# Kernel optimization log

Measured on AMD Instinct MI355X. Metric: run time of the kernel, lower is better.

The kernel has to match this reference:

```python
import jax, jax.numpy as jnp
import numpy as np

IN, H, STEPS = 4, 64, 5

def setup_inputs() -> dict:
    key = jax.random.key(0)
    ks = jax.random.split(key, 12)
    s = 1.0 / np.sqrt(H)
    def u(k, shape):
        return jax.random.uniform(k, shape, jnp.float32, -s, s)
    return {
        "x":    jax.random.normal(ks[0], (4096, 512, IN), jnp.float32),
        "Wih0": u(ks[1], (4 * H, IN)),
        "Whh0": u(ks[2], (4 * H, H)),
        "bih0": u(ks[3], (4 * H,)),
        "bhh0": u(ks[4], (4 * H,)),
        "Wih1": u(ks[5], (4 * H, H)),
        "Whh1": u(ks[6], (4 * H, H)),
        "bih1": u(ks[7], (4 * H,)),
        "bhh1": u(ks[8], (4 * H,)),
        "Wfc":  u(ks[9], (IN * STEPS, H)),
        "bfc":  u(ks[10], (IN * STEPS,)),
    }

def _lstm_layer(x, Wih, Whh, bih, bhh, collect):
    # x: [B, T, in]; PyTorch gate order: i, f, g, o
    B = x.shape[0]
    xg = jnp.einsum('bti,gi->tbg', x, Wih) + bih  # precompute input gates [T,B,4H]
    h0 = jnp.zeros((B, H), x.dtype)
    c0 = jnp.zeros((B, H), x.dtype)

    def step(carry, xg_t):
        h, c = carry
        gates = xg_t + h @ Whh.T + bhh  # [B,4H]
        i, f, g, o = jnp.split(gates, 4, axis=-1)
        i = jax.nn.sigmoid(i); f = jax.nn.sigmoid(f)
        g = jnp.tanh(g);       o = jax.nn.sigmoid(o)
        c = f * c + i * g
        h = o * jnp.tanh(c)
        return (h, c), (h if collect else None)

    (h_last, _), ys = jax.lax.scan(step, (h0, c0), xg)
    return ys, h_last  # ys: [T,B,H] (or None)

def reference(x, Wih0, Whh0, bih0, bhh0, Wih1, Whh1, bih1, bhh1, Wfc, bfc):
    ys1, _ = _lstm_layer(x, Wih0, Whh0, bih0, bhh0, collect=True)   # [T,B,H]
    x2 = jnp.transpose(ys1, (1, 0, 2))                               # [B,T,H]
    _, h_last = _lstm_layer(x2, Wih1, Whh1, bih1, bhh1, collect=False)
    out = h_last @ Wfc.T + bfc                                       # [B, IN*STEPS]
    return out.reshape(-1, STEPS, IN)
```

## Files before the change

### kernel.cpp

```cpp
#include <hip/hip_runtime.h>
#include <hip/hip_bf16.h>
#include <cstdint>

#define BLOCK 512
#define BT 16
#define RS_H 136
#define RS_F 68
#define XS   2052

typedef __attribute__((ext_vector_type(8))) short bf16x8;
typedef __attribute__((ext_vector_type(4))) float f32x4;
typedef __attribute__((ext_vector_type(2))) float f32x2;
typedef __attribute__((ext_vector_type(2))) unsigned int u32x2;

#define LOG2E 1.44269504f

static __device__ __forceinline__ float exp2_fast(float x) {
#if __has_builtin(__builtin_amdgcn_exp2f)
    return __builtin_amdgcn_exp2f(x);
#else
    return __expf(x * 0.69314718056f);
#endif
}
static __device__ __forceinline__ float rcp_fast(float x) {
    return __builtin_amdgcn_rcpf(x);
}
static __device__ __forceinline__ unsigned short f2bf(float f) {
    union { float f; unsigned u; } v; v.f = f;
    unsigned r = v.u + 0x7fffu + ((v.u >> 16) & 1u);
    return (unsigned short)(r >> 16);
}
static __device__ __forceinline__ bf16x8 load_wfrag(const float* __restrict__ w, int off, float scale) {
    union { bf16x8 v; unsigned short s[8]; } u;
#pragma unroll
    for (int j = 0; j < 8; ++j) u.s[j] = f2bf(w[off + j] * scale);
    return u.v;
}

extern "C" __global__ void __launch_bounds__(BLOCK, 2)
lstm_fused5(const float* __restrict__ x,
            const float* __restrict__ Wih0, const float* __restrict__ Whh0,
            const float* __restrict__ bih0, const float* __restrict__ bhh0,
            const float* __restrict__ Wih1, const float* __restrict__ Whh1,
            const float* __restrict__ bih1, const float* __restrict__ bhh1,
            const float* __restrict__ Wfc,  const float* __restrict__ bfc,
            float* __restrict__ out)
{
    __shared__ unsigned short hbuf[2][BT * RS_H];
    __shared__ float hfin[BT * RS_F];
    __shared__ unsigned short xlds[BT * XS + 8];

    const int tid   = threadIdx.x;
    const int b0    = blockIdx.x * BT;
    const int lane  = tid & 63;
    const int wv    = tid >> 6;
    const int layer = wv >> 2;
    const int cb    = (wv & 3) * 16;
    const int n16   = lane & 15;
    const int quad  = lane >> 4;

    for (int i = tid; i < 2 * BT * RS_H; i += BLOCK)
        ((unsigned short*)hbuf)[i] = 0;

    for (int i = tid; i < BT * 512; i += BLOCK) {
        const int r = i >> 9, t = i & 511;
        const f32x4 xv = *(const f32x4*)(x + ((size_t)(b0 + r) * 2048 + t * 4));
        const unsigned lo = (unsigned)f2bf(xv[0]) | ((unsigned)f2bf(xv[1]) << 16);
        const unsigned hi = (unsigned)f2bf(xv[2]) | ((unsigned)f2bf(xv[3]) << 16);
        *(u32x2*)&xlds[r * XS + t * 4] = (u32x2){lo, hi};
    }
    if (tid <= BT) {
        const int off = (tid < BT) ? tid * XS + 2048 : BT * XS;
        *(u32x2*)&xlds[off] = (u32x2){0u, 0u};
    }

    const float gsc[4] = {-LOG2E, -LOG2E, 2.0f * LOG2E, -LOG2E};

    bf16x8 wf[4][4];
    f32x4  biasv[4];
    if (layer == 0) {
#pragma unroll
        for (int g = 0; g < 4; ++g) {
            const int gc = g * 64 + cb + n16;
            const float s = gsc[g];
            wf[g][0] = load_wfrag(Whh0 + gc * 64, quad * 8, s);
            wf[g][1] = load_wfrag(Whh0 + gc * 64, 32 + quad * 8, s);
            union { bf16x8 v; unsigned short s_[8]; } u;
#pragma unroll
            for (int c = 0; c < 4; ++c)
                u.s_[c] = (quad == 0) ? f2bf(Wih0[gc * 4 + c] * s) : (unsigned short)0;
            u.s_[4] = 0; u.s_[5] = 0; u.s_[6] = 0; u.s_[7] = 0;
            wf[g][2] = u.v;
            const float b = (bih0[gc] + bhh0[gc]) * s;
            biasv[g] = (f32x4){b, b, b, b};
        }
    } else {
#pragma unroll
        for (int g = 0; g < 4; ++g) {
            const int gc = g * 64 + cb + n16;
            const float s = gsc[g];
            wf[g][0] = load_wfrag(Wih1 + gc * 64, quad * 8, s);
            wf[g][1] = load_wfrag(Wih1 + gc * 64, 32 + quad * 8, s);
            wf[g][2] = load_wfrag(Whh1 + gc * 64, quad * 8, s);
            wf[g][3] = load_wfrag(Whh1 + gc * 64, 32 + quad * 8, s);
            const float b = (bih1[gc] + bhh1[gc]) * s;
            biasv[g] = (f32x4){b, b, b, b};
        }
    }

    float cst[4] = {0.f, 0.f, 0.f, 0.f};

    int xoff = (quad == 0) ? n16 * XS : BT * XS;
    const int xadv = (quad == 0) ? 4 : 0;
    const int rbase = n16 * RS_H;

    const f32x2 onev  = {1.0f, 1.0f};
    const f32x2 k2l   = {2.0f * LOG2E, 2.0f * LOG2E};
    const f32x2 km2l  = {-2.0f * LOG2E, -2.0f * LOG2E};
    const f32x2 cclmp = {60.0f, 60.0f};

    __syncthreads();

    for (int it = 0; it <= 512; ++it) {
        const unsigned short* rb = &hbuf[(it + 1) & 1][0];
        unsigned short*       wb = &hbuf[it & 1][0];

        const bf16x8 a0 = *(const bf16x8*)(rb + rbase + quad * 8);
        const bf16x8 a1 = *(const bf16x8*)(rb + rbase + 32 + quad * 8);

        f32x4 acc[4];
        if (layer == 0) {
            const u32x2 xr = *(const u32x2*)&xlds[xoff];
            xoff += xadv;
            union { bf16x8 v; unsigned u[4]; } ax;
            ax.u[0] = xr.x; ax.u[1] = xr.y; ax.u[2] = 0u; ax.u[3] = 0u;
            const bf16x8 a2 = ax.v;
#pragma unroll
            for (int g = 0; g < 4; ++g) {
                acc[g] = __builtin_amdgcn_mfma_f32_16x16x32_bf16(a0, wf[g][0], biasv[g], 0, 0, 0);
                acc[g] = __builtin_amdgcn_mfma_f32_16x16x32_bf16(a1, wf[g][1], acc[g], 0, 0, 0);
                acc[g] = __builtin_amdgcn_mfma_f32_16x16x32_bf16(a2, wf[g][2], acc[g], 0, 0, 0);
            }
        } else {
            const bf16x8 a2 = *(const bf16x8*)(rb + rbase + 64 + quad * 8);
            const bf16x8 a3 = *(const bf16x8*)(rb + rbase + 96 + quad * 8);
#pragma unroll
            for (int g = 0; g < 4; ++g) {
                acc[g] = __builtin_amdgcn_mfma_f32_16x16x32_bf16(a0, wf[g][0], biasv[g], 0, 0, 0);
                acc[g] = __builtin_amdgcn_mfma_f32_16x16x32_bf16(a1, wf[g][1], acc[g], 0, 0, 0);
                acc[g] = __builtin_amdgcn_mfma_f32_16x16x32_bf16(a2, wf[g][2], acc[g], 0, 0, 0);
                acc[g] = __builtin_amdgcn_mfma_f32_16x16x32_bf16(a3, wf[g][3], acc[g], 0, 0, 0);
            }
        }

        const bool active = layer ? (it >= 1) : (it < 512);
        if (active) {
#pragma unroll
            for (int p = 0; p < 2; ++p) {
                const f32x2 ei = {exp2_fast(acc[0][2*p]), exp2_fast(acc[0][2*p+1])};
                const f32x2 ef = {exp2_fast(acc[1][2*p]), exp2_fast(acc[1][2*p+1])};
                const f32x2 eg = {exp2_fast(acc[2][2*p]), exp2_fast(acc[2][2*p+1])};
                const f32x2 eo = {exp2_fast(acc[3][2*p]), exp2_fast(acc[3][2*p+1])};

                const f32x2 t2 = __builtin_elementwise_fma(eg, k2l, km2l);
                const f32x2 d1 = (eg + onev) * (ei + onev);
                const f32x2 df = ef + onev;
                const f32x2 r1 = {rcp_fast(d1[0]), rcp_fast(d1[1])};
                const f32x2 fv = {rcp_fast(df[0]), rcp_fast(df[1])};
                const f32x2 P  = t2 * r1;

                f32x2 cp = {cst[2*p], cst[2*p+1]};
                f32x2 c2 = __builtin_elementwise_fma(fv, cp, P);
                c2 = __builtin_elementwise_min(c2, cclmp);
                cst[2*p] = c2[0]; cst[2*p+1] = c2[1];

                const f32x2 ec = {exp2_fast(c2[0]), exp2_fast(c2[1])};
                const f32x2 d2 = (ec + onev) * (eo + onev);
                const f32x2 r2 = {rcp_fast(d2[0]), rcp_fast(d2[1])};
                const f32x2 h  = (ec - onev) * r2;

                const int row0 = quad * 4 + 2 * p;
                unsigned short* wp = wb + row0 * RS_H + layer * 64 + cb + n16;
                union { __hip_bfloat162 b; unsigned short s[2]; } hb;
                hb.b = __float22bfloat162_rn(make_float2(h[0], h[1]));
                wp[0]    = hb.s[0];
                wp[RS_H] = hb.s[1];
                if (layer == 1 && it == 512) {
                    hfin[row0 * RS_F + cb + n16]       = h[0];
                    hfin[(row0 + 1) * RS_F + cb + n16] = h[1];
                }
            }
        }
        __syncthreads();
    }

    if (tid < BT * 20) {
        const int m = tid / 20, k = tid % 20;
        float acc = bfc[k];
#pragma unroll 8
        for (int j = 0; j < 64; ++j)
            acc += hfin[m * RS_F + j] * Wfc[k * 64 + j];
        out[(b0 + m) * 20 + k] = acc;
    }
}

extern "C" void kernel_launch(void* const* d_in, const int* in_sizes, int n_in,
                              void* d_out, int out_size, void* d_ws, size_t ws_size,
                              hipStream_t stream)
{
    (void)in_sizes; (void)n_in; (void)d_ws; (void)ws_size; (void)out_size;
    const float* xp    = (const float*)d_in[0];
    const float* Wih0p = (const float*)d_in[1];
    const float* Whh0p = (const float*)d_in[2];
    const float* bih0p = (const float*)d_in[3];
    const float* bhh0p = (const float*)d_in[4];
    const float* Wih1p = (const float*)d_in[5];
    const float* Whh1p = (const float*)d_in[6];
    const float* bih1p = (const float*)d_in[7];
    const float* bhh1p = (const float*)d_in[8];
    const float* Wfcp  = (const float*)d_in[9];
    const float* bfcp  = (const float*)d_in[10];

    lstm_fused5<<<dim3(256), dim3(BLOCK), 0, stream>>>(
        xp, Wih0p, Whh0p, bih0p, bhh0p, Wih1p, Whh1p, bih1p, bhh1p,
        Wfcp, bfcp, (float*)d_out);
}
```

Baseline: 432.8 us.

## Transpose MFMA operands, vectorize h stores, merge reciprocals, unroll loop by two

```diff
diff --git a/kernel.cpp b/kernel.cpp
--- a/kernel.cpp
+++ b/kernel.cpp
@@ -12,6 +12,7 @@
 typedef __attribute__((ext_vector_type(4))) float f32x4;
 typedef __attribute__((ext_vector_type(2))) float f32x2;
 typedef __attribute__((ext_vector_type(2))) unsigned int u32x2;
+typedef __attribute__((ext_vector_type(4))) unsigned int u32x4;
 
 #define LOG2E 1.44269504f
 
@@ -38,7 +39,7 @@
 }
 
 extern "C" __global__ void __launch_bounds__(BLOCK, 2)
-lstm_fused5(const float* __restrict__ x,
+lstm_fused6(const float* __restrict__ x,
             const float* __restrict__ Wih0, const float* __restrict__ Whh0,
             const float* __restrict__ bih0, const float* __restrict__ bhh0,
             const float* __restrict__ Wih1, const float* __restrict__ Whh1,
@@ -91,8 +92,10 @@
                 u.s_[c] = (quad == 0) ? f2bf(Wih0[gc * 4 + c] * s) : (unsigned short)0;
             u.s_[4] = 0; u.s_[5] = 0; u.s_[6] = 0; u.s_[7] = 0;
             wf[g][2] = u.v;
-            const float b = (bih0[gc] + bhh0[gc]) * s;
-            biasv[g] = (f32x4){b, b, b, b};
+            const int gb = g * 64 + cb + quad * 4;
+#pragma unroll
+            for (int r = 0; r < 4; ++r)
+                biasv[g][r] = (bih0[gb + r] + bhh0[gb + r]) * s;
         }
     } else {
 #pragma unroll
@@ -103,8 +106,10 @@
             wf[g][1] = load_wfrag(Wih1 + gc * 64, 32 + quad * 8, s);
             wf[g][2] = load_wfrag(Whh1 + gc * 64, quad * 8, s);
             wf[g][3] = load_wfrag(Whh1 + gc * 64, 32 + quad * 8, s);
-            const float b = (bih1[gc] + bhh1[gc]) * s;
-            biasv[g] = (f32x4){b, b, b, b};
+            const int gb = g * 64 + cb + quad * 4;
+#pragma unroll
+            for (int r = 0; r < 4; ++r)
+                biasv[g][r] = (bih1[gb + r] + bhh1[gb + r]) * s;
         }
     }
 
@@ -112,7 +117,14 @@
 
     int xoff = (quad == 0) ? n16 * XS : BT * XS;
     const int xadv = (quad == 0) ? 4 : 0;
-    const int rbase = n16 * RS_H;
+
+    const int rbase = n16 * RS_H + quad * 8;
+    const int wbase = n16 * RS_H + layer * 64 + cb + quad * 4;
+    const unsigned short* __restrict__ rdp0 = &hbuf[1][rbase];
+    const unsigned short* __restrict__ rdp1 = &hbuf[0][rbase];
+    unsigned short* __restrict__ wrp0 = &hbuf[0][wbase];
+    unsigned short* __restrict__ wrp1 = &hbuf[1][wbase];
+    float* __restrict__ hfp = &hfin[n16 * RS_F + cb + quad * 4];
 
     const f32x2 onev  = {1.0f, 1.0f};
     const f32x2 k2l   = {2.0f * LOG2E, 2.0f * LOG2E};
@@ -121,40 +133,44 @@
 
     __syncthreads();
 
-    for (int it = 0; it <= 512; ++it) {
-        const unsigned short* rb = &hbuf[(it + 1) & 1][0];
-        unsigned short*       wb = &hbuf[it & 1][0];
-
-        const bf16x8 a0 = *(const bf16x8*)(rb + rbase + quad * 8);
-        const bf16x8 a1 = *(const bf16x8*)(rb + rbase + 32 + quad * 8);
-
+    auto step = [&](const unsigned short* __restrict__ rp,
+                    unsigned short* __restrict__ wp,
+                    bool l0act, bool l1act, bool fin) __attribute__((always_inline)) {
         f32x4 acc[4];
         if (layer == 0) {
-            const u32x2 xr = *(const u32x2*)&xlds[xoff];
-            xoff += xadv;
-            union { bf16x8 v; unsigned u[4]; } ax;
-            ax.u[0] = xr.x; ax.u[1] = xr.y; ax.u[2] = 0u; ax.u[3] = 0u;
-            const bf16x8 a2 = ax.v;
-#pragma unroll
-            for (int g = 0; g < 4; ++g) {
-                acc[g] = __builtin_amdgcn_mfma_f32_16x16x32_bf16(a0, wf[g][0], biasv[g], 0, 0, 0);
-                acc[g] = __builtin_amdgcn_mfma_f32_16x16x32_bf16(a1, wf[g][1], acc[g], 0, 0, 0);
-                acc[g] = __builtin_amdgcn_mfma_f32_16x16x32_bf16(a2, wf[g][2], acc[g], 0, 0, 0);
+            if (l0act) {
+                const bf16x8 s0 = *(const bf16x8*)(rp);
+                const bf16x8 s1 = *(const bf16x8*)(rp + 32);
+                const u32x2 xr = *(const u32x2*)&xlds[xoff];
+                xoff += xadv;
+                const u32x4 xt = {xr.x, xr.y, 0u, 0u};
+                const bf16x8 sx = __builtin_bit_cast(bf16x8, xt);
+#pragma unroll
+                for (int g = 0; g < 4; ++g) {
+                    acc[g] = __builtin_amdgcn_mfma_f32_16x16x32_bf16(wf[g][0], s0, biasv[g], 0, 0, 0);
+                    acc[g] = __builtin_amdgcn_mfma_f32_16x16x32_bf16(wf[g][1], s1, acc[g], 0, 0, 0);
+                    acc[g] = __builtin_amdgcn_mfma_f32_16x16x32_bf16(wf[g][2], sx, acc[g], 0, 0, 0);
+                }
             }
         } else {
-            const bf16x8 a2 = *(const bf16x8*)(rb + rbase + 64 + quad * 8);
-            const bf16x8 a3 = *(const bf16x8*)(rb + rbase + 96 + quad * 8);
-#pragma unroll
-            for (int g = 0; g < 4; ++g) {
-                acc[g] = __builtin_amdgcn_mfma_f32_16x16x32_bf16(a0, wf[g][0], biasv[g], 0, 0, 0);
-                acc[g] = __builtin_amdgcn_mfma_f32_16x16x32_bf16(a1, wf[g][1], acc[g], 0, 0, 0);
-                acc[g] = __builtin_amdgcn_mfma_f32_16x16x32_bf16(a2, wf[g][2], acc[g], 0, 0, 0);
-                acc[g] = __builtin_amdgcn_mfma_f32_16x16x32_bf16(a3, wf[g][3], acc[g], 0, 0, 0);
+            if (l1act) {
+                const bf16x8 s0 = *(const bf16x8*)(rp);
+                const bf16x8 s1 = *(const bf16x8*)(rp + 32);
+                const bf16x8 s2 = *(const bf16x8*)(rp + 64);
+                const bf16x8 s3 = *(const bf16x8*)(rp + 96);
+#pragma unroll
+                for (int g = 0; g < 4; ++g) {
+                    acc[g] = __builtin_amdgcn_mfma_f32_16x16x32_bf16(wf[g][0], s0, biasv[g], 0, 0, 0);
+                    acc[g] = __builtin_amdgcn_mfma_f32_16x16x32_bf16(wf[g][1], s1, acc[g], 0, 0, 0);
+                    acc[g] = __builtin_amdgcn_mfma_f32_16x16x32_bf16(wf[g][2], s2, acc[g], 0, 0, 0);
+                    acc[g] = __builtin_amdgcn_mfma_f32_16x16x32_bf16(wf[g][3], s3, acc[g], 0, 0, 0);
+                }
             }
         }
-
-        const bool active = layer ? (it >= 1) : (it < 512);
-        if (active) {
+        const bool act = layer ? l1act : l0act;
+        if (act) {
+            unsigned hw0 = 0, hw1 = 0;
+            float hf0 = 0.f, hf1 = 0.f, hf2 = 0.f, hf3 = 0.f;
 #pragma unroll
             for (int p = 0; p < 2; ++p) {
                 const f32x2 ei = {exp2_fast(acc[0][2*p]), exp2_fast(acc[0][2*p+1])};
@@ -165,9 +181,10 @@
                 const f32x2 t2 = __builtin_elementwise_fma(eg, k2l, km2l);
                 const f32x2 d1 = (eg + onev) * (ei + onev);
                 const f32x2 df = ef + onev;
-                const f32x2 r1 = {rcp_fast(d1[0]), rcp_fast(d1[1])};
-                const f32x2 fv = {rcp_fast(df[0]), rcp_fast(df[1])};
-                const f32x2 P  = t2 * r1;
+                const f32x2 pr = d1 * df;
+                const f32x2 R  = {rcp_fast(pr[0]), rcp_fast(pr[1])};
+                const f32x2 P  = t2 * R * df;
+                const f32x2 fv = R * d1;
 
                 f32x2 cp = {cst[2*p], cst[2*p+1]};
                 f32x2 c2 = __builtin_elementwise_fma(fv, cp, P);
@@ -179,20 +196,25 @@
                 const f32x2 r2 = {rcp_fast(d2[0]), rcp_fast(d2[1])};
                 const f32x2 h  = (ec - onev) * r2;
 
-                const int row0 = quad * 4 + 2 * p;
-                unsigned short* wp = wb + row0 * RS_H + layer * 64 + cb + n16;
-                union { __hip_bfloat162 b; unsigned short s[2]; } hb;
+                union { __hip_bfloat162 b; unsigned u; } hb;
                 hb.b = __float22bfloat162_rn(make_float2(h[0], h[1]));
-                wp[0]    = hb.s[0];
-                wp[RS_H] = hb.s[1];
-                if (layer == 1 && it == 512) {
-                    hfin[row0 * RS_F + cb + n16]       = h[0];
-                    hfin[(row0 + 1) * RS_F + cb + n16] = h[1];
-                }
+                if (p == 0) { hw0 = hb.u; hf0 = h[0]; hf1 = h[1]; }
+                else        { hw1 = hb.u; hf2 = h[0]; hf3 = h[1]; }
             }
+            *(u32x2*)wp = (u32x2){hw0, hw1};
+            if (fin && layer == 1)
+                *(f32x4*)hfp = (f32x4){hf0, hf1, hf2, hf3};
         }
         __syncthreads();
-    }
+    };
+
+    step(rdp0, wrp0, true,  false, false);
+    for (int k = 0; k < 255; ++k) {
+        step(rdp1, wrp1, true, true, false);
+        step(rdp0, wrp0, true, true, false);
+    }
+    step(rdp1, wrp1, true,  true,  false);
+    step(rdp0, wrp0, false, true,  true);
 
     if (tid < BT * 20) {
         const int m = tid / 20, k = tid % 20;
@@ -221,7 +243,7 @@
     const float* Wfcp  = (const float*)d_in[9];
     const float* bfcp  = (const float*)d_in[10];
 
-    lstm_fused5<<<dim3(256), dim3(BLOCK), 0, stream>>>(
+    lstm_fused6<<<dim3(256), dim3(BLOCK), 0, stream>>>(
         xp, Wih0p, Whh0p, bih0p, bhh0p, Wih1p, Whh1p, bih1p, bhh1p,
         Wfcp, bfcp, (float*)d_out);
 }
```

New measurement: 417.1 us (median of 4 runs). 1.04x faster.
